# Kernel optimization log

Measured on AMD Instinct MI355X. Metric: run time of the kernel, lower is better.

The kernel has to match this reference:

```python
import jax, jax.numpy as jnp
import numpy as np

N_NODES = 100000
N_EDGES = 600000
IN_C, HID, OUT_C = 128, 256, 1

def _glorot(key, shape):
    fan_in, fan_out = shape[1], shape[0]
    lim = np.sqrt(6.0 / (fan_in + fan_out))
    return jax.random.uniform(key, shape, jnp.float32, -lim, lim)

def setup_inputs() -> dict:
    key = jax.random.key(0)
    ks = jax.random.split(key, 12)
    x = jax.random.normal(ks[0], (N_NODES, IN_C), jnp.float32)
    edge_index = jax.random.randint(ks[1], (2, N_EDGES), 0, N_NODES, jnp.int32)
    return {
        "x": x,
        "edge_index": edge_index,
        # SAGEConv1: lin_l (neighbors, with bias), lin_r (root, no bias)
        "W1l": _glorot(ks[2], (HID, IN_C)),
        "b1": jnp.zeros((HID,), jnp.float32),
        "W1r": _glorot(ks[3], (HID, IN_C)),
        # SAGEConv2
        "W2l": _glorot(ks[4], (HID, HID)),
        "b2": jnp.zeros((HID,), jnp.float32),
        "W2r": _glorot(ks[5], (HID, HID)),
        # MLP head: Linear(HID, HID//2) -> ReLU -> Linear(HID//2, OUT_C)
        "Wf1": _glorot(ks[6], (HID // 2, HID)),
        "bf1": jnp.zeros((HID // 2,), jnp.float32),
        "Wf2": _glorot(ks[7], (OUT_C, HID // 2)),
        "bf2": jnp.zeros((OUT_C,), jnp.float32),
    }

def _sage_conv(x, src, dst, Wl, b, Wr, n_nodes):
    # mean-aggregate source-node features into destination nodes
    msgs = x[src]  # [E, F] gather
    sums = jax.ops.segment_sum(msgs, dst, num_segments=n_nodes)
    cnt = jax.ops.segment_sum(jnp.ones((src.shape[0], 1), x.dtype), dst,
                              num_segments=n_nodes)
    mean = sums / jnp.maximum(cnt, 1.0)  # isolated nodes -> 0
    return mean @ Wl.T + b + x @ Wr.T

def reference(x, edge_index, W1l, b1, W1r, W2l, b2, W2r, Wf1, bf1, Wf2, bf2):
    src, dst = edge_index[0], edge_index[1]
    n = x.shape[0]
    h = jax.nn.elu(_sage_conv(x, src, dst, W1l, b1, W1r, n))
    # dropout p=0.3 is identity in eval mode
    h = jax.nn.elu(_sage_conv(h, src, dst, W2l, b2, W2r, n))
    h = jax.nn.relu(h @ Wf1.T + bf1)
    out = h @ Wf2.T + bf2  # [N, 1]
    return jnp.squeeze(out)
```

## Files before the change

kernel.cpp:

```cpp
#include <hip/hip_runtime.h>
#include <hip/hip_bf16.h>

#define NN 100000
#define NE 600000
#define NBLK 98
#define MPAD 100096

typedef __attribute__((ext_vector_type(4))) int   i32x4;
typedef __attribute__((ext_vector_type(4))) float f32x4;

__device__ __forceinline__ float b2f(unsigned short u) {
  unsigned int v = ((unsigned int)u) << 16;
  return __uint_as_float(v);
}
__device__ __forceinline__ unsigned short f2b(float f) {
  __hip_bfloat16 h = __float2bfloat16(f);
  return *reinterpret_cast<unsigned short*>(&h);
}
__device__ __forceinline__ float elu(float v) {
  return v > 0.0f ? v : (expf(v) - 1.0f);
}
__device__ __forceinline__ void gload_lds16(const void* g, void* l) {
  __builtin_amdgcn_global_load_lds(
      (const __attribute__((address_space(1))) void*)g,
      (__attribute__((address_space(3))) void*)l, 16, 0, 0);
}
__device__ __forceinline__ f32x4 mfma16(i32x4 a, i32x4 b, f32x4 c) {
  asm volatile("v_mfma_f32_16x16x32_bf16 %0, %1, %2, %0"
               : "+v"(c) : "v"(a), "v"(b));
  return c;
}

__global__ __launch_bounds__(256) void hist_kernel(
    const int* __restrict__ ei, int* __restrict__ deg) {
  const int* dst = ei + NE;
  int i = blockIdx.x * 256 + threadIdx.x;
  int n = gridDim.x * 256;
  for (int e = i; e < NE; e += n) atomicAdd(&deg[dst[e]], 1);
}

__global__ __launch_bounds__(256) void scan1_kernel(
    const int* __restrict__ deg, int* __restrict__ row, int* __restrict__ aux) {
  __shared__ int sd[256];
  int b = blockIdx.x, t = threadIdx.x;
  int base = b * 1024 + t * 4;
  int v0 = (base + 0 < NN) ? deg[base + 0] : 0;
  int v1 = (base + 1 < NN) ? deg[base + 1] : 0;
  int v2 = (base + 2 < NN) ? deg[base + 2] : 0;
  int v3 = (base + 3 < NN) ? deg[base + 3] : 0;
  int s = v0 + v1 + v2 + v3;
  sd[t] = s;
  __syncthreads();
  for (int off = 1; off < 256; off <<= 1) {
    int tmp = (t >= off) ? sd[t - off] : 0;
    __syncthreads();
    sd[t] += tmp;
    __syncthreads();
  }
  int excl = sd[t] - s;
  if (base + 0 < NN) row[base + 0] = excl;
  if (base + 1 < NN) row[base + 1] = excl + v0;
  if (base + 2 < NN) row[base + 2] = excl + v0 + v1;
  if (base + 3 < NN) row[base + 3] = excl + v0 + v1 + v2;
  if (t == 255) aux[b] = sd[t];
}

__global__ __launch_bounds__(256) void scan2_kernel(int* __restrict__ aux) {
  __shared__ int sd[256];
  int t = threadIdx.x;
  int v = (t < NBLK) ? aux[t] : 0;
  sd[t] = v;
  __syncthreads();
  for (int off = 1; off < 256; off <<= 1) {
    int tmp = (t >= off) ? sd[t - off] : 0;
    __syncthreads();
    sd[t] += tmp;
    __syncthreads();
  }
  if (t < NBLK) aux[t] = sd[t] - v;
}

__global__ __launch_bounds__(256) void scan3_kernel(
    int* __restrict__ row, const int* __restrict__ aux) {
  int i = blockIdx.x * 256 + threadIdx.x;
  if (i < NN) row[i] += aux[i >> 10];
  if (i == 0) row[NN] = NE;
}

__global__ __launch_bounds__(256) void fill_kernel(
    const int* __restrict__ ei, const int* __restrict__ row,
    int* __restrict__ cur, int* __restrict__ eidx) {
  const int* src = ei;
  const int* dst = ei + NE;
  int i = blockIdx.x * 256 + threadIdx.x;
  int n = gridDim.x * 256;
  for (int e = i; e < NE; e += n) {
    int d = dst[e];
    int p = atomicAdd(&cur[d], 1);
    eidx[row[d] + p] = src[e];
  }
}

__global__ __launch_bounds__(256) void conv_x(
    const float* __restrict__ x, unsigned short* __restrict__ A1) {
  int i = blockIdx.x * 256 + threadIdx.x;
  if (i >= NN * 32) return;
  int n = i >> 5, k4 = i & 31;
  float4 v = ((const float4*)(x + (size_t)n * 128))[k4];
  ushort4 o;
  o.x = f2b(v.x); o.y = f2b(v.y); o.z = f2b(v.z); o.w = f2b(v.w);
  ((ushort4*)(A1 + (size_t)n * 256 + 128))[k4] = o;
}

__global__ __launch_bounds__(256) void conv_w(
    const float* __restrict__ W1l, const float* __restrict__ W1r,
    const float* __restrict__ W2l, const float* __restrict__ W2r,
    const float* __restrict__ Wf1,
    unsigned short* __restrict__ W1b, unsigned short* __restrict__ W2b,
    unsigned short* __restrict__ Wf1b) {
  int i = blockIdx.x * 256 + threadIdx.x;
  const float* srcp;
  unsigned short* dstp;
  if (i < 16384) {
    int e = i * 4, j = e >> 8, k = e & 255;
    srcp = (k < 128) ? (W1l + (size_t)j * 128 + k) : (W1r + (size_t)j * 128 + (k - 128));
    dstp = W1b + e;
  } else if (i < 49152) {
    int e = (i - 16384) * 4, j = e >> 9, k = e & 511;
    srcp = (k < 256) ? (W2l + (size_t)j * 256 + k) : (W2r + (size_t)j * 256 + (k - 256));
    dstp = W2b + e;
  } else if (i < 57344) {
    int e = (i - 49152) * 4;
    srcp = Wf1 + e;
    dstp = Wf1b + e;
  } else return;
  float4 v = *(const float4*)srcp;
  ushort4 o;
  o.x = f2b(v.x); o.y = f2b(v.y); o.z = f2b(v.z); o.w = f2b(v.w);
  *(ushort4*)dstp = o;
}

__global__ __launch_bounds__(256) void agg1_csr(
    unsigned short* __restrict__ A1, const int* __restrict__ row,
    const int* __restrict__ eidx) {
  int lane = threadIdx.x & 63;
  int n = (blockIdx.x * 256 + threadIdx.x) >> 6;
  if (n >= NN) return;
  int r0 = row[n], r1 = row[n + 1];
  float ax = 0.f, ay = 0.f;
  int e = r0;
  for (; e + 1 < r1; e += 2) {
    int s0 = eidx[e], s1 = eidx[e + 1];
    ushort2 a = ((const ushort2*)(A1 + (size_t)s0 * 256 + 128))[lane];
    ushort2 b = ((const ushort2*)(A1 + (size_t)s1 * 256 + 128))[lane];
    ax += b2f(a.x) + b2f(b.x);
    ay += b2f(a.y) + b2f(b.y);
  }
  if (e < r1) {
    int s0 = eidx[e];
    ushort2 a = ((const ushort2*)(A1 + (size_t)s0 * 256 + 128))[lane];
    ax += b2f(a.x);
    ay += b2f(a.y);
  }
  float inv = 1.0f / (float)max(r1 - r0, 1);
  ushort2 o;
  o.x = f2b(ax * inv);
  o.y = f2b(ay * inv);
  ((ushort2*)(A1 + (size_t)n * 256))[lane] = o;
}

__global__ __launch_bounds__(256) void agg2_csr(
    unsigned short* __restrict__ A2, const int* __restrict__ row,
    const int* __restrict__ eidx) {
  int lane = threadIdx.x & 63;
  int n = (blockIdx.x * 256 + threadIdx.x) >> 6;
  if (n >= NN) return;
  int r0 = row[n], r1 = row[n + 1];
  float4 acc = make_float4(0.f, 0.f, 0.f, 0.f);
  int e = r0;
  for (; e + 1 < r1; e += 2) {
    int s0 = eidx[e], s1 = eidx[e + 1];
    ushort4 a = ((const ushort4*)(A2 + (size_t)s0 * 512 + 256))[lane];
    ushort4 b = ((const ushort4*)(A2 + (size_t)s1 * 512 + 256))[lane];
    acc.x += b2f(a.x) + b2f(b.x);
    acc.y += b2f(a.y) + b2f(b.y);
    acc.z += b2f(a.z) + b2f(b.z);
    acc.w += b2f(a.w) + b2f(b.w);
  }
  if (e < r1) {
    int s0 = eidx[e];
    ushort4 a = ((const ushort4*)(A2 + (size_t)s0 * 512 + 256))[lane];
    acc.x += b2f(a.x);
    acc.y += b2f(a.y);
    acc.z += b2f(a.z);
    acc.w += b2f(a.w);
  }
  float inv = 1.0f / (float)max(r1 - r0, 1);
  ushort4 o;
  o.x = f2b(acc.x * inv);
  o.y = f2b(acc.y * inv);
  o.z = f2b(acc.z * inv);
  o.w = f2b(acc.w * inv);
  ((ushort4*)(A2 + (size_t)n * 512))[lane] = o;
}

template <int K, int APITCH, int EPI>
__global__ __launch_bounds__(256) void gemm_kernel(
    const unsigned short* __restrict__ A, const unsigned short* __restrict__ Wb,
    const float* __restrict__ bias, const float* __restrict__ w2,
    const float* __restrict__ bf2p,
    unsigned short* __restrict__ Hout, int HPITCH, int HOFF,
    float* __restrict__ out) {
  __shared__ unsigned short lA[2][8192];
  __shared__ unsigned short lB[2][8192];
  int tid = threadIdx.x;
  int w = tid >> 6, lane = tid & 63;
  int lhi = lane >> 4, llo = lane & 15;
  int m0 = blockIdx.x * 128;
  int c0 = blockIdx.y * 128;
  int fb = lhi * 128 + llo * 8;

  f32x4 acc0[8], acc1[8];
#pragma unroll
  for (int n = 0; n < 8; ++n) { acc0[n] = (f32x4)0.f; acc1[n] = (f32x4)0.f; }

#define STAGE(buf, k0)                                                          \
  do {                                                                          \
    _Pragma("unroll")                                                           \
    for (int i = 0; i < 4; ++i) {                                               \
      int c = w * 4 + i;                                                        \
      int linear = c * 64 + lane;                                               \
      int r16 = linear & 15, kb = (linear >> 4) & 7, rep = linear >> 7;         \
      const unsigned short* ga =                                                \
          A + (size_t)(m0 + rep * 16 + r16) * APITCH + (k0) + kb * 8;           \
      gload_lds16(ga, &lA[buf][c * 512]);                                       \
      const unsigned short* gb =                                                \
          Wb + (size_t)(c0 + rep * 16 + r16) * K + (k0) + kb * 8;               \
      gload_lds16(gb, &lB[buf][c * 512]);                                       \
    }                                                                           \
  } while (0)

  constexpr int NSTEP = K / 64;
  STAGE(0, 0);
  asm volatile("s_waitcnt vmcnt(0)");
  __syncthreads();
  int cur = 0;
  for (int t = 0; t < NSTEP; ++t) {
    if (t + 1 < NSTEP) STAGE(cur ^ 1, (t + 1) * 64);
#pragma unroll
    for (int kc = 0; kc < 2; ++kc) {
      i32x4 a0 = *(const i32x4*)&lA[cur][(w * 2 + 0) * 1024 + kc * 512 + fb];
      i32x4 a1 = *(const i32x4*)&lA[cur][(w * 2 + 1) * 1024 + kc * 512 + fb];
#pragma unroll
      for (int n = 0; n < 8; ++n) {
        i32x4 b = *(const i32x4*)&lB[cur][n * 1024 + kc * 512 + fb];
        acc0[n] = mfma16(a0, b, acc0[n]);
        acc1[n] = mfma16(a1, b, acc1[n]);
      }
    }
    asm volatile("s_waitcnt vmcnt(0)");
    __syncthreads();
    cur ^= 1;
  }
#undef STAGE
  asm volatile("s_nop 7\n\ts_nop 7");

  if constexpr (EPI == 0) {
    float bv[8];
#pragma unroll
    for (int n = 0; n < 8; ++n) bv[n] = bias[c0 + n * 16 + llo];
#pragma unroll
    for (int mi = 0; mi < 2; ++mi) {
#pragma unroll
      for (int n = 0; n < 8; ++n) {
        f32x4 av = mi ? acc1[n] : acc0[n];
#pragma unroll
        for (int r = 0; r < 4; ++r) {
          int R = m0 + (w * 2 + mi) * 16 + lhi * 4 + r;
          float v = elu(av[r] + bv[n]);
          Hout[(size_t)R * HPITCH + HOFF + c0 + n * 16 + llo] = f2b(v);
        }
      }
    }
  } else {
    float b1v[8], w2v[8];
#pragma unroll
    for (int n = 0; n < 8; ++n) {
      b1v[n] = bias[n * 16 + llo];
      w2v[n] = w2[n * 16 + llo];
    }
    float bf2v = bf2p[0];
#pragma unroll
    for (int mi = 0; mi < 2; ++mi) {
#pragma unroll
      for (int r = 0; r < 4; ++r) {
        float s = 0.f;
#pragma unroll
        for (int n = 0; n < 8; ++n) {
          f32x4 av = mi ? acc1[n] : acc0[n];
          s += fmaxf(av[r] + b1v[n], 0.f) * w2v[n];
        }
        s += __shfl_xor(s, 1);
        s += __shfl_xor(s, 2);
        s += __shfl_xor(s, 4);
        s += __shfl_xor(s, 8);
        int R = m0 + (w * 2 + mi) * 16 + lhi * 4 + r;
        if (llo == 0 && R < NN) out[R] = s + bf2v;
      }
    }
  }
}

extern "C" void kernel_launch(void* const* d_in, const int* in_sizes, int n_in,
                              void* d_out, int out_size, void* d_ws, size_t ws_size,
                              hipStream_t stream) {
  const float* x   = (const float*)d_in[0];
  const int*   ei  = (const int*)d_in[1];
  const float* W1l = (const float*)d_in[2];
  const float* b1  = (const float*)d_in[3];
  const float* W1r = (const float*)d_in[4];
  const float* W2l = (const float*)d_in[5];
  const float* b2  = (const float*)d_in[6];
  const float* W2r = (const float*)d_in[7];
  const float* Wf1 = (const float*)d_in[8];
  const float* bf1 = (const float*)d_in[9];
  const float* Wf2 = (const float*)d_in[10];
  const float* bf2 = (const float*)d_in[11];
  float* out = (float*)d_out;

  char* ws = (char*)d_ws;
  size_t o = 0;
  int* deg = (int*)(ws + o); o += 400384;
  int* cur = (int*)(ws + o); o += 400384;
  size_t zero_bytes = o;
  int* row  = (int*)(ws + o); o += 400640;
  int* aux  = (int*)(ws + o); o += 4096;
  int* eidx = (int*)(ws + o); o += 2400000;
  unsigned short* A1 = (unsigned short*)(ws + o); o += (size_t)MPAD * 256 * 2;
  unsigned short* A2 = (unsigned short*)(ws + o); o += (size_t)MPAD * 512 * 2;
  unsigned short* h2 = (unsigned short*)(ws + o); o += (size_t)MPAD * 256 * 2;
  unsigned short* W1b  = (unsigned short*)(ws + o); o += 131072;
  unsigned short* W2b  = (unsigned short*)(ws + o); o += 262144;
  unsigned short* Wf1b = (unsigned short*)(ws + o); o += 65536;

  hipMemsetAsync(d_ws, 0, zero_bytes, stream);

  hist_kernel<<<2048, 256, 0, stream>>>(ei, deg);
  scan1_kernel<<<NBLK, 256, 0, stream>>>(deg, row, aux);
  scan2_kernel<<<1, 256, 0, stream>>>(aux);
  scan3_kernel<<<(NN + 255) / 256, 256, 0, stream>>>(row, aux);
  fill_kernel<<<2048, 256, 0, stream>>>(ei, row, cur, eidx);

  conv_x<<<(NN * 32 + 255) / 256, 256, 0, stream>>>(x, A1);
  conv_w<<<224, 256, 0, stream>>>(W1l, W1r, W2l, W2r, Wf1, W1b, W2b, Wf1b);

  agg1_csr<<<25000, 256, 0, stream>>>(A1, row, eidx);
  gemm_kernel<256, 256, 0><<<dim3(MPAD / 128, 2), 256, 0, stream>>>(
      A1, W1b, b1, nullptr, nullptr, A2, 512, 256, nullptr);
  agg2_csr<<<25000, 256, 0, stream>>>(A2, row, eidx);
  gemm_kernel<512, 512, 0><<<dim3(MPAD / 128, 2), 256, 0, stream>>>(
      A2, W2b, b2, nullptr, nullptr, h2, 256, 0, nullptr);
  gemm_kernel<256, 256, 1><<<dim3(MPAD / 128, 1), 256, 0, stream>>>(
      h2, Wf1b, bf1, Wf2, bf2, nullptr, 0, 0, out);
}
```

Measured before the change: 337.5 us.

## Fuse MLP head into conv2 GEMM, widen tiles to full N, triple-buffer loads

The second SAGE GEMM now computes all 256 output columns per block and applies ELU, stages the bf16 result in LDS, and runs the MLP head GEMM plus final dot product in the same kernel. This removes the h2 intermediate round trip and one launch. The GEMM also moves from double to triple buffering with partial vmcnt waits. The aggregation loops are unrolled by four to keep more gathers in flight. The larger accumulator set and 144KB of LDS limit occupancy to one block per CU, and the grid is halved.

Result: slower. 349.4 us (+3.5%).

```diff
diff --git a/kernel.cpp b/kernel.cpp
--- a/kernel.cpp
+++ b/kernel.cpp
@@ -30,6 +30,9 @@
                : "+v"(c) : "v"(a), "v"(b));
   return c;
 }
+#define WAITV(N) asm volatile("s_waitcnt vmcnt(" #N ")" ::: "memory")
+#define WAITALL() asm volatile("s_waitcnt vmcnt(0) lgkmcnt(0)" ::: "memory")
+#define BAR() asm volatile("s_barrier" ::: "memory")
 
 __global__ __launch_bounds__(256) void hist_kernel(
     const int* __restrict__ ei, int* __restrict__ deg) {
@@ -149,14 +152,16 @@
   int r0 = row[n], r1 = row[n + 1];
   float ax = 0.f, ay = 0.f;
   int e = r0;
-  for (; e + 1 < r1; e += 2) {
-    int s0 = eidx[e], s1 = eidx[e + 1];
+  for (; e + 3 < r1; e += 4) {
+    int s0 = eidx[e], s1 = eidx[e + 1], s2 = eidx[e + 2], s3 = eidx[e + 3];
     ushort2 a = ((const ushort2*)(A1 + (size_t)s0 * 256 + 128))[lane];
     ushort2 b = ((const ushort2*)(A1 + (size_t)s1 * 256 + 128))[lane];
-    ax += b2f(a.x) + b2f(b.x);
-    ay += b2f(a.y) + b2f(b.y);
-  }
-  if (e < r1) {
+    ushort2 c = ((const ushort2*)(A1 + (size_t)s2 * 256 + 128))[lane];
+    ushort2 d = ((const ushort2*)(A1 + (size_t)s3 * 256 + 128))[lane];
+    ax += (b2f(a.x) + b2f(b.x)) + (b2f(c.x) + b2f(d.x));
+    ay += (b2f(a.y) + b2f(b.y)) + (b2f(c.y) + b2f(d.y));
+  }
+  for (; e < r1; ++e) {
     int s0 = eidx[e];
     ushort2 a = ((const ushort2*)(A1 + (size_t)s0 * 256 + 128))[lane];
     ax += b2f(a.x);
@@ -178,16 +183,18 @@
   int r0 = row[n], r1 = row[n + 1];
   float4 acc = make_float4(0.f, 0.f, 0.f, 0.f);
   int e = r0;
-  for (; e + 1 < r1; e += 2) {
-    int s0 = eidx[e], s1 = eidx[e + 1];
+  for (; e + 3 < r1; e += 4) {
+    int s0 = eidx[e], s1 = eidx[e + 1], s2 = eidx[e + 2], s3 = eidx[e + 3];
     ushort4 a = ((const ushort4*)(A2 + (size_t)s0 * 512 + 256))[lane];
     ushort4 b = ((const ushort4*)(A2 + (size_t)s1 * 512 + 256))[lane];
-    acc.x += b2f(a.x) + b2f(b.x);
-    acc.y += b2f(a.y) + b2f(b.y);
-    acc.z += b2f(a.z) + b2f(b.z);
-    acc.w += b2f(a.w) + b2f(b.w);
-  }
-  if (e < r1) {
+    ushort4 c = ((const ushort4*)(A2 + (size_t)s2 * 512 + 256))[lane];
+    ushort4 d = ((const ushort4*)(A2 + (size_t)s3 * 512 + 256))[lane];
+    acc.x += (b2f(a.x) + b2f(b.x)) + (b2f(c.x) + b2f(d.x));
+    acc.y += (b2f(a.y) + b2f(b.y)) + (b2f(c.y) + b2f(d.y));
+    acc.z += (b2f(a.z) + b2f(b.z)) + (b2f(c.z) + b2f(d.z));
+    acc.w += (b2f(a.w) + b2f(b.w)) + (b2f(c.w) + b2f(d.w));
+  }
+  for (; e < r1; ++e) {
     int s0 = eidx[e];
     ushort4 a = ((const ushort4*)(A2 + (size_t)s0 * 512 + 256))[lane];
     acc.x += b2f(a.x);
@@ -205,91 +212,149 @@
 }
 
 template <int K, int APITCH, int EPI>
-__global__ __launch_bounds__(256) void gemm_kernel(
+__global__ __launch_bounds__(256, 1) void gemm_kernel(
     const unsigned short* __restrict__ A, const unsigned short* __restrict__ Wb,
-    const float* __restrict__ bias, const float* __restrict__ w2,
-    const float* __restrict__ bf2p,
+    const float* __restrict__ bias,
     unsigned short* __restrict__ Hout, int HPITCH, int HOFF,
+    const unsigned short* __restrict__ headW, const float* __restrict__ hb1,
+    const float* __restrict__ hw2, const float* __restrict__ hb2,
     float* __restrict__ out) {
-  __shared__ unsigned short lA[2][8192];
-  __shared__ unsigned short lB[2][8192];
+  __shared__ unsigned short lds[73728];
   int tid = threadIdx.x;
   int w = tid >> 6, lane = tid & 63;
   int lhi = lane >> 4, llo = lane & 15;
   int m0 = blockIdx.x * 128;
-  int c0 = blockIdx.y * 128;
   int fb = lhi * 128 + llo * 8;
 
-  f32x4 acc0[8], acc1[8];
-#pragma unroll
-  for (int n = 0; n < 8; ++n) { acc0[n] = (f32x4)0.f; acc1[n] = (f32x4)0.f; }
-
-#define STAGE(buf, k0)                                                          \
+  f32x4 acc0[16], acc1[16];
+#pragma unroll
+  for (int n = 0; n < 16; ++n) { acc0[n] = (f32x4)0.f; acc1[n] = (f32x4)0.f; }
+
+#define STAGE(t)                                                                \
   do {                                                                          \
+    int _be = ((t) % 3) * 24576;                                                \
+    int _k0 = (t) * 64;                                                         \
     _Pragma("unroll")                                                           \
     for (int i = 0; i < 4; ++i) {                                               \
       int c = w * 4 + i;                                                        \
       int linear = c * 64 + lane;                                               \
-      int r16 = linear & 15, kb = (linear >> 4) & 7, rep = linear >> 7;         \
       const unsigned short* ga =                                                \
-          A + (size_t)(m0 + rep * 16 + r16) * APITCH + (k0) + kb * 8;           \
-      gload_lds16(ga, &lA[buf][c * 512]);                                       \
+          A + (size_t)(m0 + (linear >> 7) * 16 + (linear & 15)) * APITCH +      \
+          _k0 + ((linear >> 4) & 7) * 8;                                        \
+      gload_lds16(ga, &lds[_be + c * 512]);                                     \
+    }                                                                           \
+    _Pragma("unroll")                                                           \
+    for (int i = 0; i < 8; ++i) {                                               \
+      int c = w * 8 + i;                                                        \
+      int linear = c * 64 + lane;                                               \
       const unsigned short* gb =                                                \
-          Wb + (size_t)(c0 + rep * 16 + r16) * K + (k0) + kb * 8;               \
-      gload_lds16(gb, &lB[buf][c * 512]);                                       \
+          Wb + (size_t)((linear >> 7) * 16 + (linear & 15)) * K +               \
+          _k0 + ((linear >> 4) & 7) * 8;                                        \
+      gload_lds16(gb, &lds[_be + 8192 + c * 512]);                              \
     }                                                                           \
   } while (0)
 
   constexpr int NSTEP = K / 64;
-  STAGE(0, 0);
-  asm volatile("s_waitcnt vmcnt(0)");
-  __syncthreads();
-  int cur = 0;
+  STAGE(0);
+  STAGE(1);
   for (int t = 0; t < NSTEP; ++t) {
-    if (t + 1 < NSTEP) STAGE(cur ^ 1, (t + 1) * 64);
+    if (t + 2 < NSTEP) {
+      STAGE(t + 2);
+      WAITV(24);
+    } else if (t + 1 < NSTEP) {
+      WAITV(12);
+    } else {
+      WAITV(0);
+    }
+    BAR();
+    const unsigned short* la = &lds[(t % 3) * 24576];
+    const unsigned short* lb = la + 8192;
 #pragma unroll
     for (int kc = 0; kc < 2; ++kc) {
-      i32x4 a0 = *(const i32x4*)&lA[cur][(w * 2 + 0) * 1024 + kc * 512 + fb];
-      i32x4 a1 = *(const i32x4*)&lA[cur][(w * 2 + 1) * 1024 + kc * 512 + fb];
-#pragma unroll
-      for (int n = 0; n < 8; ++n) {
-        i32x4 b = *(const i32x4*)&lB[cur][n * 1024 + kc * 512 + fb];
+      i32x4 a0 = *(const i32x4*)(la + (w * 2 + 0) * 1024 + kc * 512 + fb);
+      i32x4 a1 = *(const i32x4*)(la + (w * 2 + 1) * 1024 + kc * 512 + fb);
+#pragma unroll
+      for (int n = 0; n < 16; ++n) {
+        i32x4 b = *(const i32x4*)(lb + n * 1024 + kc * 512 + fb);
         acc0[n] = mfma16(a0, b, acc0[n]);
         acc1[n] = mfma16(a1, b, acc1[n]);
       }
     }
-    asm volatile("s_waitcnt vmcnt(0)");
-    __syncthreads();
-    cur ^= 1;
+    BAR();
   }
 #undef STAGE
   asm volatile("s_nop 7\n\ts_nop 7");
 
+  float bv[16];
+#pragma unroll
+  for (int n = 0; n < 16; ++n) bv[n] = bias[n * 16 + llo];
+
   if constexpr (EPI == 0) {
-    float bv[8];
-#pragma unroll
-    for (int n = 0; n < 8; ++n) bv[n] = bias[c0 + n * 16 + llo];
 #pragma unroll
     for (int mi = 0; mi < 2; ++mi) {
 #pragma unroll
-      for (int n = 0; n < 8; ++n) {
+      for (int n = 0; n < 16; ++n) {
         f32x4 av = mi ? acc1[n] : acc0[n];
 #pragma unroll
         for (int r = 0; r < 4; ++r) {
           int R = m0 + (w * 2 + mi) * 16 + lhi * 4 + r;
           float v = elu(av[r] + bv[n]);
-          Hout[(size_t)R * HPITCH + HOFF + c0 + n * 16 + llo] = f2b(v);
+          Hout[(size_t)R * HPITCH + HOFF + n * 16 + llo] = f2b(v);
         }
       }
     }
   } else {
+#pragma unroll
+    for (int i = 0; i < 16; ++i) {
+      int c = w * 16 + i;
+      int ch = c >> 4;
+      int linear = (c & 15) * 64 + lane;
+      const unsigned short* gb =
+          headW + (size_t)((linear >> 7) * 16 + (linear & 15)) * 256 +
+          ch * 64 + ((linear >> 4) & 7) * 8;
+      gload_lds16(gb, &lds[32768 + c * 512]);
+    }
+#pragma unroll
+    for (int mi = 0; mi < 2; ++mi) {
+#pragma unroll
+      for (int n = 0; n < 16; ++n) {
+        f32x4 av = mi ? acc1[n] : acc0[n];
+        int cc = n * 16 + llo;
+        int base = (cc >> 6) * 8192 + (w * 2 + mi) * 1024 +
+                   ((cc >> 3) & 7) * 128 + (cc & 7);
+#pragma unroll
+        for (int r = 0; r < 4; ++r) {
+          lds[base + (lhi * 4 + r) * 8] = f2b(elu(av[r] + bv[n]));
+        }
+      }
+    }
+    WAITALL();
+    BAR();
+    f32x4 ah0[8], ah1[8];
+#pragma unroll
+    for (int n = 0; n < 8; ++n) { ah0[n] = (f32x4)0.f; ah1[n] = (f32x4)0.f; }
+#pragma unroll
+    for (int ch = 0; ch < 4; ++ch) {
+#pragma unroll
+      for (int kc = 0; kc < 2; ++kc) {
+        i32x4 a0 = *(const i32x4*)(&lds[ch * 8192 + (w * 2 + 0) * 1024 + kc * 512 + fb]);
+        i32x4 a1 = *(const i32x4*)(&lds[ch * 8192 + (w * 2 + 1) * 1024 + kc * 512 + fb]);
+#pragma unroll
+        for (int n = 0; n < 8; ++n) {
+          i32x4 b = *(const i32x4*)(&lds[32768 + ch * 8192 + n * 1024 + kc * 512 + fb]);
+          ah0[n] = mfma16(a0, b, ah0[n]);
+          ah1[n] = mfma16(a1, b, ah1[n]);
+        }
+      }
+    }
+    asm volatile("s_nop 7\n\ts_nop 7");
     float b1v[8], w2v[8];
 #pragma unroll
     for (int n = 0; n < 8; ++n) {
-      b1v[n] = bias[n * 16 + llo];
-      w2v[n] = w2[n * 16 + llo];
-    }
-    float bf2v = bf2p[0];
+      b1v[n] = hb1[n * 16 + llo];
+      w2v[n] = hw2[n * 16 + llo];
+    }
+    float bf2v = hb2[0];
 #pragma unroll
     for (int mi = 0; mi < 2; ++mi) {
 #pragma unroll
@@ -297,7 +362,7 @@
         float s = 0.f;
 #pragma unroll
         for (int n = 0; n < 8; ++n) {
-          f32x4 av = mi ? acc1[n] : acc0[n];
+          f32x4 av = mi ? ah1[n] : ah0[n];
           s += fmaxf(av[r] + b1v[n], 0.f) * w2v[n];
         }
         s += __shfl_xor(s, 1);
@@ -338,7 +403,6 @@
   int* eidx = (int*)(ws + o); o += 2400000;
   unsigned short* A1 = (unsigned short*)(ws + o); o += (size_t)MPAD * 256 * 2;
   unsigned short* A2 = (unsigned short*)(ws + o); o += (size_t)MPAD * 512 * 2;
-  unsigned short* h2 = (unsigned short*)(ws + o); o += (size_t)MPAD * 256 * 2;
   unsigned short* W1b  = (unsigned short*)(ws + o); o += 131072;
   unsigned short* W2b  = (unsigned short*)(ws + o); o += 262144;
   unsigned short* Wf1b = (unsigned short*)(ws + o); o += 65536;
@@ -355,11 +419,9 @@
   conv_w<<<224, 256, 0, stream>>>(W1l, W1r, W2l, W2r, Wf1, W1b, W2b, Wf1b);
 
   agg1_csr<<<25000, 256, 0, stream>>>(A1, row, eidx);
-  gemm_kernel<256, 256, 0><<<dim3(MPAD / 128, 2), 256, 0, stream>>>(
-      A1, W1b, b1, nullptr, nullptr, A2, 512, 256, nullptr);
+  gemm_kernel<256, 256, 0><<<MPAD / 128, 256, 0, stream>>>(
+      A1, W1b, b1, A2, 512, 256, nullptr, nullptr, nullptr, nullptr, nullptr);
   agg2_csr<<<25000, 256, 0, stream>>>(A2, row, eidx);
-  gemm_kernel<512, 512, 0><<<dim3(MPAD / 128, 2), 256, 0, stream>>>(
-      A2, W2b, b2, nullptr, nullptr, h2, 256, 0, nullptr);
-  gemm_kernel<256, 256, 1><<<dim3(MPAD / 128, 1), 256, 0, stream>>>(
-      h2, Wf1b, bf1, Wf2, bf2, nullptr, 0, 0, out);
-}
+  gemm_kernel<512, 512, 1><<<MPAD / 128, 256, 0, stream>>>(
+      A2, W2b, b2, nullptr, 0, 0, Wf1b, bf1, Wf2, bf2, out);
+}
```

## Triple-buffer GEMM with K=32 stages and unroll CSR gather loops by four

Applied to the files above, without the earlier changes.

The GEMM moves from a double-buffered K=64 tile loop to a triple-buffered K=32 pipeline. It keeps two stages in flight and waits with partial vmcnt counts instead of draining all loads each step. It also halves LDS use and sets launch bounds to 3 blocks per CU to raise occupancy. The aggregation kernels now gather four neighbor rows per iteration instead of two, exposing more memory-level parallelism. The cost is two barriers per smaller step and more register pressure in the gather loops.

New measurement: 319.7 us. -5.3%, faster.

```diff
diff --git a/kernel.cpp b/kernel.cpp
--- a/kernel.cpp
+++ b/kernel.cpp
@@ -30,6 +30,8 @@
                : "+v"(c) : "v"(a), "v"(b));
   return c;
 }
+#define WAITV(N) asm volatile("s_waitcnt vmcnt(" #N ")" ::: "memory")
+#define BAR() asm volatile("s_barrier" ::: "memory")
 
 __global__ __launch_bounds__(256) void hist_kernel(
     const int* __restrict__ ei, int* __restrict__ deg) {
@@ -149,14 +151,16 @@
   int r0 = row[n], r1 = row[n + 1];
   float ax = 0.f, ay = 0.f;
   int e = r0;
-  for (; e + 1 < r1; e += 2) {
-    int s0 = eidx[e], s1 = eidx[e + 1];
+  for (; e + 3 < r1; e += 4) {
+    int s0 = eidx[e], s1 = eidx[e + 1], s2 = eidx[e + 2], s3 = eidx[e + 3];
     ushort2 a = ((const ushort2*)(A1 + (size_t)s0 * 256 + 128))[lane];
     ushort2 b = ((const ushort2*)(A1 + (size_t)s1 * 256 + 128))[lane];
-    ax += b2f(a.x) + b2f(b.x);
-    ay += b2f(a.y) + b2f(b.y);
-  }
-  if (e < r1) {
+    ushort2 c = ((const ushort2*)(A1 + (size_t)s2 * 256 + 128))[lane];
+    ushort2 d = ((const ushort2*)(A1 + (size_t)s3 * 256 + 128))[lane];
+    ax += (b2f(a.x) + b2f(b.x)) + (b2f(c.x) + b2f(d.x));
+    ay += (b2f(a.y) + b2f(b.y)) + (b2f(c.y) + b2f(d.y));
+  }
+  for (; e < r1; ++e) {
     int s0 = eidx[e];
     ushort2 a = ((const ushort2*)(A1 + (size_t)s0 * 256 + 128))[lane];
     ax += b2f(a.x);
@@ -178,16 +182,18 @@
   int r0 = row[n], r1 = row[n + 1];
   float4 acc = make_float4(0.f, 0.f, 0.f, 0.f);
   int e = r0;
-  for (; e + 1 < r1; e += 2) {
-    int s0 = eidx[e], s1 = eidx[e + 1];
+  for (; e + 3 < r1; e += 4) {
+    int s0 = eidx[e], s1 = eidx[e + 1], s2 = eidx[e + 2], s3 = eidx[e + 3];
     ushort4 a = ((const ushort4*)(A2 + (size_t)s0 * 512 + 256))[lane];
     ushort4 b = ((const ushort4*)(A2 + (size_t)s1 * 512 + 256))[lane];
-    acc.x += b2f(a.x) + b2f(b.x);
-    acc.y += b2f(a.y) + b2f(b.y);
-    acc.z += b2f(a.z) + b2f(b.z);
-    acc.w += b2f(a.w) + b2f(b.w);
-  }
-  if (e < r1) {
+    ushort4 c = ((const ushort4*)(A2 + (size_t)s2 * 512 + 256))[lane];
+    ushort4 d = ((const ushort4*)(A2 + (size_t)s3 * 512 + 256))[lane];
+    acc.x += (b2f(a.x) + b2f(b.x)) + (b2f(c.x) + b2f(d.x));
+    acc.y += (b2f(a.y) + b2f(b.y)) + (b2f(c.y) + b2f(d.y));
+    acc.z += (b2f(a.z) + b2f(b.z)) + (b2f(c.z) + b2f(d.z));
+    acc.w += (b2f(a.w) + b2f(b.w)) + (b2f(c.w) + b2f(d.w));
+  }
+  for (; e < r1; ++e) {
     int s0 = eidx[e];
     ushort4 a = ((const ushort4*)(A2 + (size_t)s0 * 512 + 256))[lane];
     acc.x += b2f(a.x);
@@ -205,62 +211,65 @@
 }
 
 template <int K, int APITCH, int EPI>
-__global__ __launch_bounds__(256) void gemm_kernel(
+__global__ __launch_bounds__(256, 3) void gemm_kernel(
     const unsigned short* __restrict__ A, const unsigned short* __restrict__ Wb,
     const float* __restrict__ bias, const float* __restrict__ w2,
     const float* __restrict__ bf2p,
     unsigned short* __restrict__ Hout, int HPITCH, int HOFF,
     float* __restrict__ out) {
-  __shared__ unsigned short lA[2][8192];
-  __shared__ unsigned short lB[2][8192];
+  __shared__ unsigned short lA[3][4096];
+  __shared__ unsigned short lB[3][4096];
   int tid = threadIdx.x;
   int w = tid >> 6, lane = tid & 63;
   int lhi = lane >> 4, llo = lane & 15;
   int m0 = blockIdx.x * 128;
   int c0 = blockIdx.y * 128;
-  int fb = lhi * 128 + llo * 8;
+  int fb = lane * 8;
 
   f32x4 acc0[8], acc1[8];
 #pragma unroll
   for (int n = 0; n < 8; ++n) { acc0[n] = (f32x4)0.f; acc1[n] = (f32x4)0.f; }
 
-#define STAGE(buf, k0)                                                          \
+#define STAGE(t)                                                                \
   do {                                                                          \
+    int _b = (t) % 3;                                                           \
+    int _k0 = (t) * 32;                                                         \
     _Pragma("unroll")                                                           \
-    for (int i = 0; i < 4; ++i) {                                               \
-      int c = w * 4 + i;                                                        \
-      int linear = c * 64 + lane;                                               \
-      int r16 = linear & 15, kb = (linear >> 4) & 7, rep = linear >> 7;         \
+    for (int i = 0; i < 2; ++i) {                                               \
+      int c = w * 2 + i;                                                        \
       const unsigned short* ga =                                                \
-          A + (size_t)(m0 + rep * 16 + r16) * APITCH + (k0) + kb * 8;           \
-      gload_lds16(ga, &lA[buf][c * 512]);                                       \
+          A + (size_t)(m0 + c * 16 + llo) * APITCH + _k0 + lhi * 8;             \
+      gload_lds16(ga, &lA[_b][c * 512]);                                        \
       const unsigned short* gb =                                                \
-          Wb + (size_t)(c0 + rep * 16 + r16) * K + (k0) + kb * 8;               \
-      gload_lds16(gb, &lB[buf][c * 512]);                                       \
+          Wb + (size_t)(c0 + c * 16 + llo) * K + _k0 + lhi * 8;                 \
+      gload_lds16(gb, &lB[_b][c * 512]);                                        \
     }                                                                           \
   } while (0)
 
-  constexpr int NSTEP = K / 64;
-  STAGE(0, 0);
-  asm volatile("s_waitcnt vmcnt(0)");
-  __syncthreads();
-  int cur = 0;
+  constexpr int NSTEP = K / 32;
+  STAGE(0);
+  STAGE(1);
   for (int t = 0; t < NSTEP; ++t) {
-    if (t + 1 < NSTEP) STAGE(cur ^ 1, (t + 1) * 64);
-#pragma unroll
-    for (int kc = 0; kc < 2; ++kc) {
-      i32x4 a0 = *(const i32x4*)&lA[cur][(w * 2 + 0) * 1024 + kc * 512 + fb];
-      i32x4 a1 = *(const i32x4*)&lA[cur][(w * 2 + 1) * 1024 + kc * 512 + fb];
-#pragma unroll
-      for (int n = 0; n < 8; ++n) {
-        i32x4 b = *(const i32x4*)&lB[cur][n * 1024 + kc * 512 + fb];
-        acc0[n] = mfma16(a0, b, acc0[n]);
-        acc1[n] = mfma16(a1, b, acc1[n]);
-      }
-    }
-    asm volatile("s_waitcnt vmcnt(0)");
-    __syncthreads();
-    cur ^= 1;
+    if (t + 2 < NSTEP) {
+      STAGE(t + 2);
+      WAITV(8);
+    } else if (t + 1 < NSTEP) {
+      WAITV(4);
+    } else {
+      WAITV(0);
+    }
+    BAR();
+    const unsigned short* la = &lA[t % 3][0];
+    const unsigned short* lb = &lB[t % 3][0];
+    i32x4 a0 = *(const i32x4*)(la + (w * 2 + 0) * 512 + fb);
+    i32x4 a1 = *(const i32x4*)(la + (w * 2 + 1) * 512 + fb);
+#pragma unroll
+    for (int n = 0; n < 8; ++n) {
+      i32x4 b = *(const i32x4*)(lb + n * 512 + fb);
+      acc0[n] = mfma16(a0, b, acc0[n]);
+      acc1[n] = mfma16(a1, b, acc1[n]);
+    }
+    BAR();
   }
 #undef STAGE
   asm volatile("s_nop 7\n\ts_nop 7");
```
